# Optimization experiments

Measured on AMD Instinct MI355X. Metric: run time of the kernel, lower is better.

## Reference

```python
import jax, jax.numpy as jnp
import numpy as np

N_NODES = 20000
N_EDGES = 320000
L = 128
NODE_IN = 30
EDGE_IN = 4
NUM_LAYERS = 5


def _mlp(x, w1, b1, a, w2, b2):
    # Linear -> PReLU(scalar slope) -> Linear
    h = x @ w1 + b1
    h = jnp.where(h > 0, h, a * h)
    return h @ w2 + b2


def setup_inputs() -> dict:
    key = jax.random.key(0)
    ks = iter(jax.random.split(key, 64))
    s = 0.02

    def w(shape):
        return (s * jax.random.normal(next(ks), shape)).astype(jnp.float32)

    inp = {}
    inp["x"] = jax.random.normal(next(ks), (N_NODES, NODE_IN), dtype=jnp.float32)
    inp["edge_attr"] = jax.random.normal(next(ks), (N_EDGES, EDGE_IN), dtype=jnp.float32)
    inp["edge_index"] = jax.random.randint(next(ks), (2, N_EDGES), 0, N_NODES, dtype=jnp.int32)
    # node encoder
    inp["ne_w1"] = w((NODE_IN, L)); inp["ne_b1"] = jnp.zeros((L,), jnp.float32)
    inp["ne_a"] = jnp.float32(0.25)
    inp["ne_w2"] = w((L, L)); inp["ne_b2"] = jnp.zeros((L,), jnp.float32)
    # edge encoder
    inp["ee_w1"] = w((EDGE_IN, L)); inp["ee_b1"] = jnp.zeros((L,), jnp.float32)
    inp["ee_a"] = jnp.float32(0.25)
    inp["ee_w2"] = w((L, L)); inp["ee_b2"] = jnp.zeros((L,), jnp.float32)
    # processor layers (stacked over NUM_LAYERS)
    inp["le_w1"] = w((NUM_LAYERS, 3 * L, L)); inp["le_b1"] = jnp.zeros((NUM_LAYERS, L), jnp.float32)
    inp["le_a"] = jnp.full((NUM_LAYERS,), 0.25, jnp.float32)
    inp["le_w2"] = w((NUM_LAYERS, L, L)); inp["le_b2"] = jnp.zeros((NUM_LAYERS, L), jnp.float32)
    inp["ln_w1"] = w((NUM_LAYERS, 2 * L, L)); inp["ln_b1"] = jnp.zeros((NUM_LAYERS, L), jnp.float32)
    inp["ln_a"] = jnp.full((NUM_LAYERS,), 0.25, jnp.float32)
    inp["ln_w2"] = w((NUM_LAYERS, L, L)); inp["ln_b2"] = jnp.zeros((NUM_LAYERS, L), jnp.float32)
    # decoder
    inp["de_w1"] = w((L, L)); inp["de_b1"] = jnp.zeros((L,), jnp.float32)
    inp["de_a"] = jnp.float32(0.25)
    inp["de_w2"] = w((L, 3)); inp["de_b2"] = jnp.zeros((3,), jnp.float32)
    return inp


def reference(x, edge_attr, edge_index,
              ne_w1, ne_b1, ne_a, ne_w2, ne_b2,
              ee_w1, ee_b1, ee_a, ee_w2, ee_b2,
              le_w1, le_b1, le_a, le_w2, le_b2,
              ln_w1, ln_b1, ln_a, ln_w2, ln_b2,
              de_w1, de_b1, de_a, de_w2, de_b2):
    n = x.shape[0]
    src = edge_index[0]  # x_j (source)
    dst = edge_index[1]  # x_i (target), aggregation index

    h = _mlp(x, ne_w1, ne_b1, ne_a, ne_w2, ne_b2)            # [N, L]
    e = _mlp(edge_attr, ee_w1, ee_b1, ee_a, ee_w2, ee_b2)    # [E, L]

    for l in range(le_w1.shape[0]):
        m = jnp.concatenate([h[dst], h[src], e], axis=-1)    # [E, 3L]
        m = _mlp(m, le_w1[l], le_b1[l], le_a[l], le_w2[l], le_b2[l])  # [E, L]
        agg = jax.ops.segment_sum(m, dst, num_segments=n)    # [N, L]
        upd = _mlp(jnp.concatenate([h, agg], axis=-1),
                   ln_w1[l], ln_b1[l], ln_a[l], ln_w2[l], ln_b2[l])
        h = h + upd

    return _mlp(h, de_w1, de_b1, de_a, de_w2, de_b2)         # [N, 3]
```

## Files before the change

### kernel.cpp

```cpp
#include <hip/hip_runtime.h>
#include <cstdint>
#include <cstddef>


#define DEVI static __device__ __forceinline__

typedef __bf16 bf16_t;
typedef bf16_t bf16x8 __attribute__((ext_vector_type(8)));
typedef bf16_t bf16x4 __attribute__((ext_vector_type(4)));
typedef float f32x4v __attribute__((ext_vector_type(4)));

DEVI float4 ld4(const float* p) { return *(const float4*)p; }
DEVI void st4(float* p, float4 v) { *(float4*)p = v; }
DEVI float prelu1(float z, float a) { return z > 0.f ? z : a * z; }
DEVI void atomicAddF(float* p, float v) {
  __hip_atomic_fetch_add(p, v, __ATOMIC_RELAXED, __HIP_MEMORY_SCOPE_AGENT);
}
DEVI f32x4v mfma_bf16(bf16x8 a, bf16x8 b, f32x4v c) {
  return __builtin_amdgcn_mfma_f32_16x16x32_bf16(a, b, c, 0, 0, 0);
}
DEVI void mfma3(f32x4v& acc, bf16x8 ah, bf16x8 al, bf16x8 bh, bf16x8 bl) {
  acc = mfma_bf16(ah, bh, acc);
  acc = mfma_bf16(al, bh, acc);
  acc = mfma_bf16(ah, bl, acc);
}
DEVI void split2(float x, bf16_t& h, bf16_t& l) {
  h = (bf16_t)x;
  l = (bf16_t)(x - (float)h);
}
DEVI bf16x8 ldb8(const bf16_t* p) { return *(const bf16x8*)p; }

#define NST 136
#define EST 72


DEVI void stage_f32(const float* __restrict__ src, int row0, int M,
                    int lane, int wave, bf16_t* SAh, bf16_t* SAl)
{
  const int row = wave * 16 + (lane >> 2);
  const int grow = row0 + row;
  const int colbase = (lane & 3) * 32;
  #pragma unroll
  for (int j = 0; j < 8; ++j) {
    int kc = colbase + j * 4;
    float4 v = make_float4(0.f, 0.f, 0.f, 0.f);
    if (grow < M) v = ld4(src + (size_t)grow * 128 + kc);
    bf16_t h0,l0,h1,l1,h2,l2,h3,l3;
    split2(v.x,h0,l0); split2(v.y,h1,l1); split2(v.z,h2,l2); split2(v.w,h3,l3);
    *(bf16x4*)(SAh + row * NST + kc) = (bf16x4){h0,h1,h2,h3};
    *(bf16x4*)(SAl + row * NST + kc) = (bf16x4){l0,l1,l2,l3};
  }
}

DEVI void stage_planes(const bf16_t* __restrict__ gh, const bf16_t* __restrict__ gl,
                       int row0, int M, int lane, int wave,
                       bf16_t* SAh, bf16_t* SAl)
{
  const int row = wave * 16 + (lane >> 2);
  const int grow = row0 + row;
  const int colbase = (lane & 3) * 32;
  #pragma unroll
  for (int j = 0; j < 4; ++j) {
    int kc = colbase + j * 8;
    bf16x8 vh = {};
    bf16x8 vl = {};
    if (grow < M) {
      vh = ldb8(gh + (size_t)grow * 128 + kc);
      vl = ldb8(gl + (size_t)grow * 128 + kc);
    }
    *(bf16x8*)(SAh + row * NST + kc) = vh;
    *(bf16x8*)(SAl + row * NST + kc) = vl;
  }
}

DEVI void gemm_lds(const bf16_t* SAh, const bf16_t* SAl,
                   const bf16_t* __restrict__ BT, f32x4v acc[8],
                   int wave, int p, int q)
{
  #pragma unroll
  for (int ks = 0; ks < 4; ++ks) {
    const int k0 = ks * 32 + q * 8;
    bf16x8 aH = ldb8(SAh + (wave * 16 + p) * NST + k0);
    bf16x8 aL = ldb8(SAl + (wave * 16 + p) * NST + k0);
    #pragma unroll
    for (int nt = 0; nt < 8; ++nt) {
      const bf16_t* bp = BT + (size_t)(nt * 16 + p) * 128 + k0;
      mfma3(acc[nt], aH, aL, ldb8(bp), ldb8(bp + 16384));
    }
  }
}

DEVI void store_c(float* __restrict__ O, int row0, int M,
                  const f32x4v acc[8], int wave, int p, int q)
{
  int rb = row0 + wave * 16 + q * 4;
  #pragma unroll
  for (int r = 0; r < 4; ++r) {
    if (rb + r < M) {
      float* op = O + (size_t)(rb + r) * 128 + p * 8;
      st4(op,     make_float4(acc[0][r], acc[1][r], acc[2][r], acc[3][r]));
      st4(op + 4, make_float4(acc[4][r], acc[5][r], acc[6][r], acc[7][r]));
    }
  }
}

DEVI void stage_cregs(const f32x4v acc[8], int wave, int p, int q,
                      bf16_t* SAh, bf16_t* SAl)
{
  #pragma unroll
  for (int r = 0; r < 4; ++r) {
    int row = wave * 16 + q * 4 + r;
    bf16x8 vh, vl;
    #pragma unroll
    for (int nt = 0; nt < 8; ++nt) {
      bf16_t hb, lb;
      split2(acc[nt][r], hb, lb);
      vh[nt] = hb; vl[nt] = lb;
    }
    *(bf16x8*)(SAh + row * NST + p * 8) = vh;
    *(bf16x8*)(SAl + row * NST + p * 8) = vl;
  }
}

DEVI void planes_out(bf16_t* __restrict__ gh, bf16_t* __restrict__ gl,
                     int row0, int M, int lane, int wave,
                     const bf16_t* SAh, const bf16_t* SAl)
{
  const int row = wave * 16 + (lane >> 2);
  const int grow = row0 + row;
  const int colbase = (lane & 3) * 32;
  if (grow < M) {
    #pragma unroll
    for (int j = 0; j < 4; ++j) {
      int kc = colbase + j * 8;
      *(bf16x8*)(gh + (size_t)grow * 128 + kc) = *(const bf16x8*)(SAh + row * NST + kc);
      *(bf16x8*)(gl + (size_t)grow * 128 + kc) = *(const bf16x8*)(SAl + row * NST + kc);
    }
  }
}

DEVI void ld8f(float dst[8], const float* __restrict__ src, int p) {
  *(float4*)(dst)     = ld4(src + p * 8);
  *(float4*)(dst + 4) = ld4(src + p * 8 + 4);
}

__global__ __launch_bounds__(128, 2) void k_svu(
    float* Sbuf,
    bf16_t* __restrict__ hSh, bf16_t* __restrict__ hSl,
    const bf16_t* __restrict__ WtilT, const bf16_t* __restrict__ Wn1aT,
    const bf16_t* __restrict__ lnw2T, const bf16_t* __restrict__ W1nextT,
    const float* __restrict__ ln_b1_l, const float* __restrict__ btil_l,
    const int* __restrict__ deg, const float* __restrict__ ln_a_l,
    const float* __restrict__ ln_b2_l,
    float* __restrict__ P, float* __restrict__ Q, int doPQ, int M)
{
  __shared__ __align__(16) bf16_t SAh[32 * NST];
  __shared__ __align__(16) bf16_t SAl[32 * NST];
  const int t = threadIdx.x, lane = t & 63, wave = t >> 6;
  const int p = lane & 15, q = lane >> 4;
  const int row0 = blockIdx.x * 32;

  f32x4v acc1[8];
  #pragma unroll
  for (int j = 0; j < 8; ++j) acc1[j] = (f32x4v){0.f, 0.f, 0.f, 0.f};

  stage_f32(Sbuf, row0, M, lane, wave, SAh, SAl);
  {
    const int row = wave * 16 + (lane >> 2);
    const int grow = row0 + row;
    const int colbase = (lane & 3) * 32;
    if (grow < M) {
      float4 z4 = make_float4(0.f, 0.f, 0.f, 0.f);
      #pragma unroll
      for (int j = 0; j < 8; ++j)
        st4(Sbuf + (size_t)grow * 128 + colbase + j * 4, z4);
    }
  }
  gemm_lds(SAh, SAl, WtilT, acc1, wave, p, q);
  stage_planes(hSh, hSl, row0, M, lane, wave, SAh, SAl);
  gemm_lds(SAh, SAl, Wn1aT, acc1, wave, p, q);

  float hold[8][4];
  #pragma unroll
  for (int r = 0; r < 4; ++r) {
    int row = wave * 16 + q * 4 + r;
    bf16x8 vh = *(const bf16x8*)(SAh + row * NST + p * 8);
    bf16x8 vl = *(const bf16x8*)(SAl + row * NST + p * 8);
    #pragma unroll
    for (int nt = 0; nt < 8; ++nt)
      hold[nt][r] = (float)vh[nt] + (float)vl[nt];
  }
  const float alpha = *ln_a_l;
  float degf[4];
  #pragma unroll
  for (int r = 0; r < 4; ++r) {
    int row = row0 + wave * 16 + q * 4 + r;
    degf[r] = (row < M) ? (float)deg[row] : 0.f;
  }
  float b1c[8], btc[8];
  ld8f(b1c, ln_b1_l, p);
  ld8f(btc, btil_l, p);
  #pragma unroll
  for (int nt = 0; nt < 8; ++nt)
    #pragma unroll
    for (int r = 0; r < 4; ++r)
      acc1[nt][r] = prelu1(acc1[nt][r] + b1c[nt] + degf[r] * btc[nt], alpha);

  stage_cregs(acc1, wave, p, q, SAh, SAl);
  f32x4v acc2[8];
  #pragma unroll
  for (int j = 0; j < 8; ++j) acc2[j] = (f32x4v){0.f, 0.f, 0.f, 0.f};
  gemm_lds(SAh, SAl, lnw2T, acc2, wave, p, q);
  float b2c[8];
  ld8f(b2c, ln_b2_l, p);
  #pragma unroll
  for (int nt = 0; nt < 8; ++nt)
    #pragma unroll
    for (int r = 0; r < 4; ++r)
      acc2[nt][r] = hold[nt][r] + acc2[nt][r] + b2c[nt];

  stage_cregs(acc2, wave, p, q, SAh, SAl);
  planes_out(hSh, hSl, row0, M, lane, wave, SAh, SAl);

  if (doPQ) {
    f32x4v acc3[8];
    #pragma unroll
    for (int j = 0; j < 8; ++j) acc3[j] = (f32x4v){0.f, 0.f, 0.f, 0.f};
    gemm_lds(SAh, SAl, W1nextT, acc3, wave, p, q);
    store_c(P, row0, M, acc3, wave, p, q);
    #pragma unroll
    for (int j = 0; j < 8; ++j) acc3[j] = (f32x4v){0.f, 0.f, 0.f, 0.f};
    gemm_lds(SAh, SAl, W1nextT + 32768, acc3, wave, p, q);
    store_c(Q, row0, M, acc3, wave, p, q);
  }
}

__global__ __launch_bounds__(128, 2) void k_enc(
    const float* __restrict__ UN, const bf16_t* __restrict__ new2T,
    const float* __restrict__ b2, const bf16_t* __restrict__ W1T0,
    bf16_t* __restrict__ hSh, bf16_t* __restrict__ hSl,
    float* __restrict__ P, float* __restrict__ Q, int M)
{
  __shared__ __align__(16) bf16_t SAh[32 * NST];
  __shared__ __align__(16) bf16_t SAl[32 * NST];
  const int t = threadIdx.x, lane = t & 63, wave = t >> 6;
  const int p = lane & 15, q = lane >> 4;
  const int row0 = blockIdx.x * 32;

  f32x4v acc[8];
  #pragma unroll
  for (int j = 0; j < 8; ++j) acc[j] = (f32x4v){0.f, 0.f, 0.f, 0.f};
  stage_f32(UN, row0, M, lane, wave, SAh, SAl);
  gemm_lds(SAh, SAl, new2T, acc, wave, p, q);
  float b2c[8];
  ld8f(b2c, b2, p);
  #pragma unroll
  for (int nt = 0; nt < 8; ++nt)
    #pragma unroll
    for (int r = 0; r < 4; ++r) acc[nt][r] += b2c[nt];
  stage_cregs(acc, wave, p, q, SAh, SAl);
  planes_out(hSh, hSl, row0, M, lane, wave, SAh, SAl);

  f32x4v acc3[8];
  #pragma unroll
  for (int j = 0; j < 8; ++j) acc3[j] = (f32x4v){0.f, 0.f, 0.f, 0.f};
  gemm_lds(SAh, SAl, W1T0, acc3, wave, p, q);
  store_c(P, row0, M, acc3, wave, p, q);
  #pragma unroll
  for (int j = 0; j < 8; ++j) acc3[j] = (f32x4v){0.f, 0.f, 0.f, 0.f};
  gemm_lds(SAh, SAl, W1T0 + 32768, acc3, wave, p, q);
  store_c(Q, row0, M, acc3, wave, p, q);
}

__global__ __launch_bounds__(256, 3) void k_edge(
    const float* __restrict__ sEa, const int* __restrict__ sSrc,
    const int* __restrict__ sDst,
    const int* __restrict__ rowStart, const int* __restrict__ deg,
    const float* __restrict__ ee_w1, const float* __restrict__ ee_b1,
    const float* __restrict__ ee_a,
    const bf16_t* __restrict__ WhatT, const float* __restrict__ bvec,
    const float* __restrict__ alpha_ptr,
    const float* __restrict__ P, const float* __restrict__ Q,
    float* __restrict__ S, int N, int E)
{
  __shared__ __align__(16) float Stile[32 * 132];
  __shared__ __align__(16) float ew[640];
  __shared__ __align__(16) bf16_t Ast[128 * EST];

  const int t = threadIdx.x, lane = t & 63, wave = t >> 6;
  const int p = lane & 15, q = lane >> 4;
  const int e0 = blockIdx.x * 128;
  const int dstLo = sDst[e0];

  for (int i = t; i < 640; i += 256)
    ew[i] = (i < 512) ? ee_w1[i] : ee_b1[i - 512];
  for (int i = t; i < 32 * 132; i += 256) Stile[i] = 0.f;
  __syncthreads();

  const float ua = *ee_a;
  const float alpha = *alpha_ptr;
  float bvc[8];
  ld8f(bvc, bvec, p);

  const int srow = wave * 32 + (lane >> 1);
  const int scb = (lane & 1) * 32;
  float4 eav = make_float4(0.f, 0.f, 0.f, 0.f);
  {
    int ed = e0 + srow;
    if (ed < E) eav = ld4(sEa + (size_t)ed * 4);
  }

  f32x4v acc[2][8];
  #pragma unroll
  for (int i = 0; i < 2; ++i)
    #pragma unroll
    for (int j = 0; j < 8; ++j) acc[i][j] = (f32x4v){0.f, 0.f, 0.f, 0.f};

  for (int c = 0; c < 2; ++c) {
    #pragma unroll
    for (int j = 0; j < 8; ++j) {
      int kc = scb + j * 4;
      int kg = c * 64 + kc;
      float4 w0 = ld4(ew + kg);
      float4 w1 = ld4(ew + 128 + kg);
      float4 w2 = ld4(ew + 256 + kg);
      float4 w3 = ld4(ew + 384 + kg);
      float4 bb = ld4(ew + 512 + kg);
      float ux = bb.x, uy = bb.y, uz = bb.z, uw = bb.w;
      ux = fmaf(eav.x, w0.x, ux); uy = fmaf(eav.x, w0.y, uy);
      uz = fmaf(eav.x, w0.z, uz); uw = fmaf(eav.x, w0.w, uw);
      ux = fmaf(eav.y, w1.x, ux); uy = fmaf(eav.y, w1.y, uy);
      uz = fmaf(eav.y, w1.z, uz); uw = fmaf(eav.y, w1.w, uw);
      ux = fmaf(eav.z, w2.x, ux); uy = fmaf(eav.z, w2.y, uy);
      uz = fmaf(eav.z, w2.z, uz); uw = fmaf(eav.z, w2.w, uw);
      ux = fmaf(eav.w, w3.x, ux); uy = fmaf(eav.w, w3.y, uy);
      uz = fmaf(eav.w, w3.z, uz); uw = fmaf(eav.w, w3.w, uw);
      *(bf16x4*)(Ast + srow * EST + kc) = (bf16x4){
          (bf16_t)prelu1(ux, ua), (bf16_t)prelu1(uy, ua),
          (bf16_t)prelu1(uz, ua), (bf16_t)prelu1(uw, ua)};
    }
    #pragma unroll
    for (int ks = 0; ks < 2; ++ks) {
      const int k0 = ks * 32 + q * 8;
      const int kg = c * 64 + k0;
      bf16x8 aH0 = ldb8(Ast + (wave * 32 + p) * EST + k0);
      bf16x8 aH1 = ldb8(Ast + (wave * 32 + 16 + p) * EST + k0);
      #pragma unroll
      for (int nt = 0; nt < 8; ++nt) {
        const bf16_t* bp = WhatT + (size_t)(nt * 16 + p) * 128 + kg;
        bf16x8 bH = ldb8(bp);
        bf16x8 bL = ldb8(bp + 16384);
        acc[0][nt] = mfma_bf16(aH0, bH, acc[0][nt]);
        acc[0][nt] = mfma_bf16(aH0, bL, acc[0][nt]);
        acc[1][nt] = mfma_bf16(aH1, bH, acc[1][nt]);
        acc[1][nt] = mfma_bf16(aH1, bL, acc[1][nt]);
      }
    }
  }

  #pragma unroll
  for (int mt = 0; mt < 2; ++mt) {
    float rs[8];
    #pragma unroll
    for (int nt = 0; nt < 8; ++nt) rs[nt] = 0.f;
    int curd = -1;
    float pv[8];
    #pragma unroll
    for (int nt = 0; nt < 8; ++nt) pv[nt] = 0.f;
    #pragma unroll
    for (int r = 0; r < 4; ++r) {
      int ed = e0 + wave * 32 + mt * 16 + q * 4 + r;
      if (ed < E) {
        int d = sDst[ed];
        int s = sSrc[ed];
        if (d != curd) {
          if (curd >= 0) {
            int rr = curd - dstLo;
            if (rr < 32) {
              #pragma unroll
              for (int nt = 0; nt < 8; ++nt)
                atomicAdd(&Stile[rr * 132 + p * 8 + nt], rs[nt]);
            } else {
              #pragma unroll
              for (int nt = 0; nt < 8; ++nt)
                atomicAddF(S + (size_t)curd * 128 + p * 8 + nt, rs[nt]);
            }
            #pragma unroll
            for (int nt = 0; nt < 8; ++nt) rs[nt] = 0.f;
          }
          curd = d;
          ld8f(pv, P + (size_t)d * 128, p);
          #pragma unroll
          for (int nt = 0; nt < 8; ++nt) pv[nt] += bvc[nt];
        }
        float qv[8];
        ld8f(qv, Q + (size_t)s * 128, p);
        #pragma unroll
        for (int nt = 0; nt < 8; ++nt) {
          float z = acc[mt][nt][r] + pv[nt] + qv[nt];
          rs[nt] += prelu1(z, alpha);
        }
      }
    }
    if (curd >= 0) {
      int rr = curd - dstLo;
      if (rr < 32) {
        #pragma unroll
        for (int nt = 0; nt < 8; ++nt)
          atomicAdd(&Stile[rr * 132 + p * 8 + nt], rs[nt]);
      } else {
        #pragma unroll
        for (int nt = 0; nt < 8; ++nt)
          atomicAddF(S + (size_t)curd * 128 + p * 8 + nt, rs[nt]);
      }
    }
  }
  __syncthreads();

  const int lastE = (e0 + 127 < E) ? (e0 + 127) : (E - 1);
  const int dstHi = sDst[lastE];
  const int col4 = (t & 31) * 4;
  #pragma unroll
  for (int rr0 = 0; rr0 < 32; rr0 += 8) {
    int rr = rr0 + (t >> 5);
    int d = dstLo + rr;
    if (d <= dstHi && d < N) {
      float4 v = ld4(&Stile[rr * 132 + col4]);
      bool interior = (rowStart[d] >= e0) && (rowStart[d] + deg[d] <= e0 + 128);
      float* sp = S + (size_t)d * 128 + col4;
      if (interior) {
        st4(sp, v);
      } else {
        atomicAddF(sp + 0, v.x); atomicAddF(sp + 1, v.y);
        atomicAddF(sp + 2, v.z); atomicAddF(sp + 3, v.w);
      }
    }
  }
}

__global__ __launch_bounds__(128, 4) void k_dec(
    const bf16_t* __restrict__ hSh, const bf16_t* __restrict__ hSl,
    const bf16_t* __restrict__ dw1T,
    const float* __restrict__ de_b1, const float* __restrict__ de_a,
    const float* __restrict__ de_w2, const float* __restrict__ de_b2,
    float* __restrict__ out, int M)
{
  __shared__ __align__(16) float Cs[32][132];
  __shared__ __align__(16) float w2s[384];
  const int t = threadIdx.x, lane = t & 63, wave = t >> 6;
  const int p = lane & 15, q = lane >> 4;
  const int row0 = blockIdx.x * 32;
  for (int i = t; i < 384; i += 128) w2s[i] = de_w2[i];

  f32x4v acc[8];
  #pragma unroll
  for (int j = 0; j < 8; ++j) acc[j] = (f32x4v){0.f, 0.f, 0.f, 0.f};
  const size_t ra = (size_t)(row0 + wave * 16 + p) * 128;
  #pragma unroll
  for (int ks = 0; ks < 4; ++ks) {
    const int k0 = ks * 32 + q * 8;
    bf16x8 aH = ldb8(hSh + ra + k0);
    bf16x8 aL = ldb8(hSl + ra + k0);
    #pragma unroll
    for (int nt = 0; nt < 8; ++nt) {
      const bf16_t* bp = dw1T + (size_t)(nt * 16 + p) * 128 + k0;
      mfma3(acc[nt], aH, aL, ldb8(bp), ldb8(bp + 16384));
    }
  }
  const float alpha = *de_a;
  float b1c[8];
  ld8f(b1c, de_b1, p);
  #pragma unroll
  for (int r = 0; r < 4; ++r) {
    int row = wave * 16 + q * 4 + r;
    float* cp = &Cs[row][p * 8];
    st4(cp, make_float4(prelu1(acc[0][r] + b1c[0], alpha),
                        prelu1(acc[1][r] + b1c[1], alpha),
                        prelu1(acc[2][r] + b1c[2], alpha),
                        prelu1(acc[3][r] + b1c[3], alpha)));
    st4(cp + 4, make_float4(prelu1(acc[4][r] + b1c[4], alpha),
                            prelu1(acc[5][r] + b1c[5], alpha),
                            prelu1(acc[6][r] + b1c[6], alpha),
                            prelu1(acc[7][r] + b1c[7], alpha)));
  }
  __syncthreads();
  if (t < 32) {
    float s0 = de_b2[0], s1 = de_b2[1], s2 = de_b2[2];
    for (int k = 0; k < 128; ++k) {
      float vv = Cs[t][k];
      s0 = fmaf(vv, w2s[k * 3 + 0], s0);
      s1 = fmaf(vv, w2s[k * 3 + 1], s1);
      s2 = fmaf(vv, w2s[k * 3 + 2], s2);
    }
    int row = row0 + t;
    if (row < M) {
      out[(size_t)row * 3 + 0] = s0;
      out[(size_t)row * 3 + 1] = s1;
      out[(size_t)row * 3 + 2] = s2;
    }
  }
}

__global__ __launch_bounds__(256) void k_tsplit(
    const float* __restrict__ ne_w2, const float* __restrict__ de_w1,
    const float* __restrict__ le_w1, const float* __restrict__ ln_w1,
    const float* __restrict__ ln_w2, bf16_t* __restrict__ WT)
{
  int jid = blockIdx.x;
  const float* src; int slot;
  if (jid == 0)      { src = ne_w2; slot = 0; }
  else if (jid == 1) { src = de_w1; slot = 1; }
  else {
    int l = (jid - 2) >> 2, wj = (jid - 2) & 3;
    slot = 2 + l * 6 + wj;
    src = (wj == 0) ? le_w1 + (size_t)l * 49152
        : (wj == 1) ? le_w1 + (size_t)l * 49152 + 16384
        : (wj == 2) ? ln_w1 + (size_t)l * 32768
                    : ln_w2 + (size_t)l * 16384;
  }
  bf16_t* oh = WT + (size_t)slot * 32768;
  bf16_t* ol = oh + 16384;
  for (int idx = threadIdx.x; idx < 16384; idx += 256) {
    int k = idx >> 7, n = idx & 127;
    bf16_t hb, lb;
    split2(src[idx], hb, lb);
    int pos = ((n & 7) * 16 + (n >> 3)) * 128 + k;
    oh[pos] = hb;
    ol[pos] = lb;
  }
}

__global__ __launch_bounds__(256) void k_fold(
    const float* __restrict__ ee_w2, const float* __restrict__ ee_b2,
    const float* __restrict__ le_w1, const float* __restrict__ le_b1,
    const float* __restrict__ le_w2, const float* __restrict__ le_b2,
    const float* __restrict__ ln_w1,
    bf16_t* __restrict__ WT, float* __restrict__ bvec, float* __restrict__ btil)
{
  const int l = blockIdx.x;
  const int which = blockIdx.y;
  const int z = blockIdx.z;
  const float* L; const float* Rm; const float* lb; const float* badd;
  int slot; float* bout;
  if (which == 0) {
    L = ee_w2; Rm = le_w1 + (size_t)l * 49152 + 256 * 128;
    lb = ee_b2; badd = le_b1 + l * 128;
    slot = 2 + l * 6 + 4; bout = bvec + l * 128;
  } else {
    L = le_w2 + (size_t)l * 16384; Rm = ln_w1 + (size_t)l * 32768 + 128 * 128;
    lb = le_b2 + l * 128; badd = nullptr;
    slot = 2 + l * 6 + 5; bout = btil + l * 128;
  }
  bf16_t* oh = WT + (size_t)slot * 32768;
  bf16_t* ol = oh + 16384;
  const int t = threadIdx.x;
  const int base = z * 2048;
  for (int eidx = base + t; eidx < base + 2048; eidx += 256) {
    int k = eidx >> 7, n = eidx & 127;
    float a = 0.f;
    for (int d = 0; d < 128; d += 4) {
      float4 lv = ld4(L + k * 128 + d);
      a = fmaf(lv.x, Rm[(d + 0) * 128 + n], a);
      a = fmaf(lv.y, Rm[(d + 1) * 128 + n], a);
      a = fmaf(lv.z, Rm[(d + 2) * 128 + n], a);
      a = fmaf(lv.w, Rm[(d + 3) * 128 + n], a);
    }
    bf16_t hb, lbv;
    split2(a, hb, lbv);
    int pos = ((n & 7) * 16 + (n >> 3)) * 128 + k;
    oh[pos] = hb;
    ol[pos] = lbv;
  }
  if (z == 0 && t < 128) {
    float a = badd ? badd[t] : 0.f;
    for (int d = 0; d < 128; ++d) a = fmaf(lb[d], Rm[d * 128 + t], a);
    bout[t] = a;
  }
}

__global__ __launch_bounds__(256) void k_node_u(
    const float* __restrict__ x, const float* __restrict__ w1,
    const float* __restrict__ b1, const float* __restrict__ a_ptr,
    float* __restrict__ U, int M)
{
  int gid = blockIdx.x * 256 + threadIdx.x;
  int m = gid >> 5;
  if (m >= M) return;
  int nc = (gid & 31) << 2;
  float a = *a_ptr;
  float4 bb = ld4(b1 + nc);
  float z0 = bb.x, z1 = bb.y, z2 = bb.z, z3 = bb.w;
  const float* xr = x + (size_t)m * 30;
  #pragma unroll
  for (int j = 0; j < 30; ++j) {
    float xv = xr[j];
    float4 wv = ld4(w1 + j * 128 + nc);
    z0 = fmaf(xv, wv.x, z0); z1 = fmaf(xv, wv.y, z1);
    z2 = fmaf(xv, wv.z, z2); z3 = fmaf(xv, wv.w, z3);
  }
  st4(U + (size_t)m * 128 + nc,
      make_float4(prelu1(z0, a), prelu1(z1, a), prelu1(z2, a), prelu1(z3, a)));
}

__global__ void k_hist(const int* __restrict__ dstIdx, int* __restrict__ deg, int E) {
  int i = blockIdx.x * 256 + threadIdx.x;
  if (i < E) atomicAdd(deg + dstIdx[i], 1);
}

__global__ __launch_bounds__(1024) void k_scan(
    const int* __restrict__ deg, int* __restrict__ cursor,
    int* __restrict__ rowStart, int N, int per)
{
  __shared__ int part[1024];
  const int t = threadIdx.x;
  const int base = t * per;
  int local = 0;
  for (int i = 0; i < per; ++i) {
    int idx = base + i;
    if (idx < N) local += deg[idx];
  }
  part[t] = local;
  __syncthreads();
  for (int off = 1; off < 1024; off <<= 1) {
    int v = (t >= off) ? part[t - off] : 0;
    __syncthreads();
    part[t] += v;
    __syncthreads();
  }
  int run = (t == 0) ? 0 : part[t - 1];
  for (int i = 0; i < per; ++i) {
    int idx = base + i;
    if (idx < N) {
      cursor[idx] = run;
      rowStart[idx] = run;
      run += deg[idx];
    }
  }
}

__global__ void k_scatter(const int* __restrict__ srcIdx, const int* __restrict__ dstIdx,
                          const float* __restrict__ ea, int* __restrict__ cursor,
                          int* __restrict__ sSrc, int* __restrict__ sDst,
                          float* __restrict__ sEa, int E)
{
  int e = blockIdx.x * 256 + threadIdx.x;
  if (e < E) {
    int d = dstIdx[e];
    int p = atomicAdd(cursor + d, 1);
    sSrc[p] = srcIdx[e];
    sDst[p] = d;
    st4(sEa + (size_t)p * 4, ld4(ea + (size_t)e * 4));
  }
}

extern "C" void kernel_launch(void* const* d_in, const int* in_sizes, int n_in,
                              void* d_out, int out_size, void* d_ws, size_t ws_size,
                              hipStream_t stream)
{
  const float* x     = (const float*)d_in[0];
  const float* ea    = (const float*)d_in[1];
  const int*   ei    = (const int*)  d_in[2];
  const float* ne_w1 = (const float*)d_in[3];
  const float* ne_b1 = (const float*)d_in[4];
  const float* ne_a  = (const float*)d_in[5];
  const float* ne_w2 = (const float*)d_in[6];
  const float* ne_b2 = (const float*)d_in[7];
  const float* ee_w1 = (const float*)d_in[8];
  const float* ee_b1 = (const float*)d_in[9];
  const float* ee_a  = (const float*)d_in[10];
  const float* ee_w2 = (const float*)d_in[11];
  const float* ee_b2 = (const float*)d_in[12];
  const float* le_w1 = (const float*)d_in[13];
  const float* le_b1 = (const float*)d_in[14];
  const float* le_a  = (const float*)d_in[15];
  const float* le_w2 = (const float*)d_in[16];
  const float* le_b2 = (const float*)d_in[17];
  const float* ln_w1 = (const float*)d_in[18];
  const float* ln_b1 = (const float*)d_in[19];
  const float* ln_a  = (const float*)d_in[20];
  const float* ln_w2 = (const float*)d_in[21];
  const float* ln_b2 = (const float*)d_in[22];
  const float* de_w1 = (const float*)d_in[23];
  const float* de_b1 = (const float*)d_in[24];
  const float* de_a  = (const float*)d_in[25];
  const float* de_w2 = (const float*)d_in[26];
  const float* de_b2 = (const float*)d_in[27];

  const int N = in_sizes[0] / 30;
  const int E = in_sizes[1] / 4;
  const int* srcIdx = ei;
  const int* dstIdx = ei + E;

  const int g32 = (N + 31) / 32;
  const int gE  = (E + 127) / 128;
  const int Np = g32 * 32;
  const size_t NNp = (size_t)Np * 128;

  float* w = (float*)d_ws;
  float* Pb   = w; w += NNp;
  float* Qb   = w; w += NNp;
  float* Sb   = w; w += NNp;
  float* bvec = w; w += 5 * 128;
  float* btil = w; w += 5 * 128;
  float* sEa  = w; w += (size_t)E * 4;
  bf16_t* hSh = (bf16_t*)w;
  bf16_t* hSl = hSh + NNp;  w += NNp;
  bf16_t* WT  = (bf16_t*)w; w += 32 * 32768 / 2;
  int* ip     = (int*)w;
  int* deg    = ip; ip += N;
  int* cursor = ip; ip += N;
  int* rowStart = ip; ip += N;
  int* sSrc   = ip; ip += E;
  int* sDst   = ip; ip += E;

  float* out = (float*)d_out;

  k_tsplit<<<dim3(22), dim3(256), 0, stream>>>(ne_w2, de_w1, le_w1, ln_w1, ln_w2, WT);
  k_fold<<<dim3(5, 2, 8), dim3(256), 0, stream>>>(ee_w2, ee_b2, le_w1, le_b1,
                                                  le_w2, le_b2, ln_w1, WT, bvec, btil);
  hipMemsetAsync(deg, 0, (size_t)N * 4, stream);
  k_hist<<<dim3((E + 255) / 256), dim3(256), 0, stream>>>(dstIdx, deg, E);
  k_scan<<<dim3(1), dim3(1024), 0, stream>>>(deg, cursor, rowStart, N,
                                             (N + 1023) / 1024);
  k_scatter<<<dim3((E + 255) / 256), dim3(256), 0, stream>>>(
      srcIdx, dstIdx, ea, cursor, sSrc, sDst, sEa, E);

  k_node_u<<<dim3((N * 32 + 255) / 256), dim3(256), 0, stream>>>(x, ne_w1, ne_b1, ne_a, Sb, N);
  k_enc<<<dim3(g32), dim3(128), 0, stream>>>(Sb, WT, ne_b2, WT + 2 * 32768,
                                             hSh, hSl, Pb, Qb, N);

  hipMemsetAsync(Sb, 0, (size_t)N * 128 * 4, stream);

  for (int l = 0; l < 5; ++l) {
    const bf16_t* slotL = WT + (size_t)(2 + l * 6) * 32768;
    k_edge<<<dim3(gE), dim3(256), 0, stream>>>(
        sEa, sSrc, sDst, rowStart, deg, ee_w1, ee_b1, ee_a,
        slotL + 4 * 32768, bvec + l * 128, le_a + l, Pb, Qb, Sb, N, E);
    const bf16_t* W1next = (l < 4) ? (WT + (size_t)(2 + (l + 1) * 6) * 32768) : WT;
    k_svu<<<dim3(g32), dim3(128), 0, stream>>>(
        Sb, hSh, hSl, slotL + 5 * 32768, slotL + 2 * 32768, slotL + 3 * 32768,
        W1next, ln_b1 + (size_t)l * 128, btil + l * 128, deg, ln_a + l,
        ln_b2 + (size_t)l * 128, Pb, Qb, (l < 4) ? 1 : 0, N);
  }

  k_dec<<<dim3(g32), dim3(128), 0, stream>>>(hSh, hSl, WT + 32768, de_b1, de_a,
                                             de_w2, de_b2, out, N);
}
```

Baseline: 1.396 ms.

## Split node-update GEMM columns across four waves per 32-row block

The node-update and encoder kernels move from 2 waves (each owning 16 rows and all 128 output columns) to 4 waves, where each wave owns 16 rows and half of the output columns. Accumulator count per thread halves, and the staging, store and LDS split helpers are rewritten for the half-width layout. Because waves now share rows in LDS, __syncthreads barriers are added between staging and GEMM phases. The aim is more wave parallelism and lower register pressure on the node-side kernels, at the cost of extra barriers and each wave reloading its A fragments.

```diff
diff --git a/kernel.cpp b/kernel.cpp
--- a/kernel.cpp
+++ b/kernel.cpp
@@ -34,14 +34,14 @@
 #define EST 72
 
 
-DEVI void stage_f32(const float* __restrict__ src, int row0, int M,
-                    int lane, int wave, bf16_t* SAh, bf16_t* SAl)
-{
-  const int row = wave * 16 + (lane >> 2);
+DEVI void stage_f32_c4(const float* __restrict__ src, int row0, int M,
+                       int lane, int h, int cH, bf16_t* SAh, bf16_t* SAl)
+{
+  const int row = h * 16 + (lane >> 2);
   const int grow = row0 + row;
-  const int colbase = (lane & 3) * 32;
-  #pragma unroll
-  for (int j = 0; j < 8; ++j) {
+  const int colbase = cH * 64 + (lane & 3) * 16;
+  #pragma unroll
+  for (int j = 0; j < 4; ++j) {
     int kc = colbase + j * 4;
     float4 v = make_float4(0.f, 0.f, 0.f, 0.f);
     if (grow < M) v = ld4(src + (size_t)grow * 128 + kc);
@@ -52,15 +52,15 @@
   }
 }
 
-DEVI void stage_planes(const bf16_t* __restrict__ gh, const bf16_t* __restrict__ gl,
-                       int row0, int M, int lane, int wave,
-                       bf16_t* SAh, bf16_t* SAl)
-{
-  const int row = wave * 16 + (lane >> 2);
+DEVI void stage_planes_c4(const bf16_t* __restrict__ gh, const bf16_t* __restrict__ gl,
+                          int row0, int M, int lane, int h, int cH,
+                          bf16_t* SAh, bf16_t* SAl)
+{
+  const int row = h * 16 + (lane >> 2);
   const int grow = row0 + row;
-  const int colbase = (lane & 3) * 32;
-  #pragma unroll
-  for (int j = 0; j < 4; ++j) {
+  const int colbase = cH * 64 + (lane & 3) * 16;
+  #pragma unroll
+  for (int j = 0; j < 2; ++j) {
     int kc = colbase + j * 8;
     bf16x8 vh = {};
     bf16x8 vl = {};
@@ -73,65 +73,64 @@
   }
 }
 
-DEVI void gemm_lds(const bf16_t* SAh, const bf16_t* SAl,
-                   const bf16_t* __restrict__ BT, f32x4v acc[8],
-                   int wave, int p, int q)
+DEVI void gemm_c4(const bf16_t* SAh, const bf16_t* SAl,
+                  const bf16_t* __restrict__ BT, f32x4v acc[4],
+                  int h, int ntb, int p, int q)
 {
   #pragma unroll
   for (int ks = 0; ks < 4; ++ks) {
     const int k0 = ks * 32 + q * 8;
-    bf16x8 aH = ldb8(SAh + (wave * 16 + p) * NST + k0);
-    bf16x8 aL = ldb8(SAl + (wave * 16 + p) * NST + k0);
-    #pragma unroll
-    for (int nt = 0; nt < 8; ++nt) {
-      const bf16_t* bp = BT + (size_t)(nt * 16 + p) * 128 + k0;
+    bf16x8 aH = ldb8(SAh + (h * 16 + p) * NST + k0);
+    bf16x8 aL = ldb8(SAl + (h * 16 + p) * NST + k0);
+    #pragma unroll
+    for (int nt = 0; nt < 4; ++nt) {
+      const bf16_t* bp = BT + (size_t)((ntb + nt) * 16 + p) * 128 + k0;
       mfma3(acc[nt], aH, aL, ldb8(bp), ldb8(bp + 16384));
     }
   }
 }
 
-DEVI void store_c(float* __restrict__ O, int row0, int M,
-                  const f32x4v acc[8], int wave, int p, int q)
-{
-  int rb = row0 + wave * 16 + q * 4;
+DEVI void store_c4(float* __restrict__ O, int row0, int M,
+                   const f32x4v acc[4], int h, int cH, int p, int q)
+{
+  int rb = row0 + h * 16 + q * 4;
   #pragma unroll
   for (int r = 0; r < 4; ++r) {
     if (rb + r < M) {
-      float* op = O + (size_t)(rb + r) * 128 + p * 8;
-      st4(op,     make_float4(acc[0][r], acc[1][r], acc[2][r], acc[3][r]));
-      st4(op + 4, make_float4(acc[4][r], acc[5][r], acc[6][r], acc[7][r]));
-    }
-  }
-}
-
-DEVI void stage_cregs(const f32x4v acc[8], int wave, int p, int q,
-                      bf16_t* SAh, bf16_t* SAl)
+      float* op = O + (size_t)(rb + r) * 128 + p * 8 + cH * 4;
+      st4(op, make_float4(acc[0][r], acc[1][r], acc[2][r], acc[3][r]));
+    }
+  }
+}
+
+DEVI void stage_cregs_c4(const f32x4v acc[4], int h, int cH, int p, int q,
+                         bf16_t* SAh, bf16_t* SAl)
 {
   #pragma unroll
   for (int r = 0; r < 4; ++r) {
-    int row = wave * 16 + q * 4 + r;
-    bf16x8 vh, vl;
-    #pragma unroll
-    for (int nt = 0; nt < 8; ++nt) {
+    int row = h * 16 + q * 4 + r;
+    bf16x4 vh, vl;
+    #pragma unroll
+    for (int nt = 0; nt < 4; ++nt) {
       bf16_t hb, lb;
       split2(acc[nt][r], hb, lb);
       vh[nt] = hb; vl[nt] = lb;
     }
-    *(bf16x8*)(SAh + row * NST + p * 8) = vh;
-    *(bf16x8*)(SAl + row * NST + p * 8) = vl;
-  }
-}
-
-DEVI void planes_out(bf16_t* __restrict__ gh, bf16_t* __restrict__ gl,
-                     int row0, int M, int lane, int wave,
-                     const bf16_t* SAh, const bf16_t* SAl)
-{
-  const int row = wave * 16 + (lane >> 2);
+    *(bf16x4*)(SAh + row * NST + p * 8 + cH * 4) = vh;
+    *(bf16x4*)(SAl + row * NST + p * 8 + cH * 4) = vl;
+  }
+}
+
+DEVI void planes_out_c4(bf16_t* __restrict__ gh, bf16_t* __restrict__ gl,
+                        int row0, int M, int lane, int h, int cH,
+                        const bf16_t* SAh, const bf16_t* SAl)
+{
+  const int row = h * 16 + (lane >> 2);
   const int grow = row0 + row;
-  const int colbase = (lane & 3) * 32;
+  const int colbase = cH * 64 + (lane & 3) * 16;
   if (grow < M) {
     #pragma unroll
-    for (int j = 0; j < 4; ++j) {
+    for (int j = 0; j < 2; ++j) {
       int kc = colbase + j * 8;
       *(bf16x8*)(gh + (size_t)grow * 128 + kc) = *(const bf16x8*)(SAh + row * NST + kc);
       *(bf16x8*)(gl + (size_t)grow * 128 + kc) = *(const bf16x8*)(SAl + row * NST + kc);
@@ -144,7 +143,11 @@
   *(float4*)(dst + 4) = ld4(src + p * 8 + 4);
 }
 
-__global__ __launch_bounds__(128, 2) void k_svu(
+DEVI void ld4f(float dst[4], const float* __restrict__ src, int p, int cH) {
+  *(float4*)(dst) = ld4(src + p * 8 + cH * 4);
+}
+
+__global__ __launch_bounds__(256, 2) void k_svu(
     float* Sbuf,
     bf16_t* __restrict__ hSh, bf16_t* __restrict__ hSl,
     const bf16_t* __restrict__ WtilT, const bf16_t* __restrict__ Wn1aT,
@@ -157,85 +160,95 @@
   __shared__ __align__(16) bf16_t SAh[32 * NST];
   __shared__ __align__(16) bf16_t SAl[32 * NST];
   const int t = threadIdx.x, lane = t & 63, wave = t >> 6;
+  const int h = wave & 1, cH = wave >> 1;
   const int p = lane & 15, q = lane >> 4;
   const int row0 = blockIdx.x * 32;
 
-  f32x4v acc1[8];
-  #pragma unroll
-  for (int j = 0; j < 8; ++j) acc1[j] = (f32x4v){0.f, 0.f, 0.f, 0.f};
-
-  stage_f32(Sbuf, row0, M, lane, wave, SAh, SAl);
+  f32x4v acc1[4];
+  #pragma unroll
+  for (int j = 0; j < 4; ++j) acc1[j] = (f32x4v){0.f, 0.f, 0.f, 0.f};
+
+  stage_f32_c4(Sbuf, row0, M, lane, h, cH, SAh, SAl);
   {
-    const int row = wave * 16 + (lane >> 2);
+    const int row = h * 16 + (lane >> 2);
     const int grow = row0 + row;
-    const int colbase = (lane & 3) * 32;
+    const int colbase = cH * 64 + (lane & 3) * 16;
     if (grow < M) {
       float4 z4 = make_float4(0.f, 0.f, 0.f, 0.f);
       #pragma unroll
-      for (int j = 0; j < 8; ++j)
+      for (int j = 0; j < 4; ++j)
         st4(Sbuf + (size_t)grow * 128 + colbase + j * 4, z4);
     }
   }
-  gemm_lds(SAh, SAl, WtilT, acc1, wave, p, q);
-  stage_planes(hSh, hSl, row0, M, lane, wave, SAh, SAl);
-  gemm_lds(SAh, SAl, Wn1aT, acc1, wave, p, q);
-
-  float hold[8][4];
+  __syncthreads();
+  gemm_c4(SAh, SAl, WtilT, acc1, h, cH * 4, p, q);
+  __syncthreads();
+  stage_planes_c4(hSh, hSl, row0, M, lane, h, cH, SAh, SAl);
+  __syncthreads();
+  gemm_c4(SAh, SAl, Wn1aT, acc1, h, cH * 4, p, q);
+
+  float hold[4][4];
   #pragma unroll
   for (int r = 0; r < 4; ++r) {
-    int row = wave * 16 + q * 4 + r;
-    bf16x8 vh = *(const bf16x8*)(SAh + row * NST + p * 8);
-    bf16x8 vl = *(const bf16x8*)(SAl + row * NST + p * 8);
-    #pragma unroll
-    for (int nt = 0; nt < 8; ++nt)
+    int row = h * 16 + q * 4 + r;
+    bf16x4 vh = *(const bf16x4*)(SAh + row * NST + p * 8 + cH * 4);
+    bf16x4 vl = *(const bf16x4*)(SAl + row * NST + p * 8 + cH * 4);
+    #pragma unroll
+    for (int nt = 0; nt < 4; ++nt)
       hold[nt][r] = (float)vh[nt] + (float)vl[nt];
   }
+  __syncthreads();
+
   const float alpha = *ln_a_l;
   float degf[4];
   #pragma unroll
   for (int r = 0; r < 4; ++r) {
-    int row = row0 + wave * 16 + q * 4 + r;
+    int row = row0 + h * 16 + q * 4 + r;
     degf[r] = (row < M) ? (float)deg[row] : 0.f;
   }
-  float b1c[8], btc[8];
-  ld8f(b1c, ln_b1_l, p);
-  ld8f(btc, btil_l, p);
-  #pragma unroll
-  for (int nt = 0; nt < 8; ++nt)
+  float b1c[4], btc[4];
+  ld4f(b1c, ln_b1_l, p, cH);
+  ld4f(btc, btil_l, p, cH);
+  #pragma unroll
+  for (int nt = 0; nt < 4; ++nt)
     #pragma unroll
     for (int r = 0; r < 4; ++r)
       acc1[nt][r] = prelu1(acc1[nt][r] + b1c[nt] + degf[r] * btc[nt], alpha);
 
-  stage_cregs(acc1, wave, p, q, SAh, SAl);
-  f32x4v acc2[8];
-  #pragma unroll
-  for (int j = 0; j < 8; ++j) acc2[j] = (f32x4v){0.f, 0.f, 0.f, 0.f};
-  gemm_lds(SAh, SAl, lnw2T, acc2, wave, p, q);
-  float b2c[8];
-  ld8f(b2c, ln_b2_l, p);
-  #pragma unroll
-  for (int nt = 0; nt < 8; ++nt)
+  stage_cregs_c4(acc1, h, cH, p, q, SAh, SAl);
+  __syncthreads();
+  f32x4v acc2[4];
+  #pragma unroll
+  for (int j = 0; j < 4; ++j) acc2[j] = (f32x4v){0.f, 0.f, 0.f, 0.f};
+  gemm_c4(SAh, SAl, lnw2T, acc2, h, cH * 4, p, q);
+  __syncthreads();
+
+  float b2c[4];
+  ld4f(b2c, ln_b2_l, p, cH);
+  #pragma unroll
+  for (int nt = 0; nt < 4; ++nt)
     #pragma unroll
     for (int r = 0; r < 4; ++r)
       acc2[nt][r] = hold[nt][r] + acc2[nt][r] + b2c[nt];
 
-  stage_cregs(acc2, wave, p, q, SAh, SAl);
-  planes_out(hSh, hSl, row0, M, lane, wave, SAh, SAl);
+  stage_cregs_c4(acc2, h, cH, p, q, SAh, SAl);
+  __syncthreads();
+  planes_out_c4(hSh, hSl, row0, M, lane, h, cH, SAh, SAl);
 
   if (doPQ) {
-    f32x4v acc3[8];
-    #pragma unroll
-    for (int j = 0; j < 8; ++j) acc3[j] = (f32x4v){0.f, 0.f, 0.f, 0.f};
-    gemm_lds(SAh, SAl, W1nextT, acc3, wave, p, q);
-    store_c(P, row0, M, acc3, wave, p, q);
-    #pragma unroll
-    for (int j = 0; j < 8; ++j) acc3[j] = (f32x4v){0.f, 0.f, 0.f, 0.f};
-    gemm_lds(SAh, SAl, W1nextT + 32768, acc3, wave, p, q);
-    store_c(Q, row0, M, acc3, wave, p, q);
-  }
-}
-
-__global__ __launch_bounds__(128, 2) void k_enc(
+    f32x4v acc3[4];
+    #pragma unroll
+    for (int j = 0; j < 4; ++j) acc3[j] = (f32x4v){0.f, 0.f, 0.f, 0.f};
+    gemm_c4(SAh, SAl, W1nextT, acc3, h, cH * 4, p, q);
+    store_c4(P, row0, M, acc3, h, cH, p, q);
+    #pragma unroll
+    for (int j = 0; j < 4; ++j) acc3[j] = (f32x4v){0.f, 0.f, 0.f, 0.f};
+    gemm_c4(SAh, SAl, W1nextT + 32768, acc3, h, cH * 4, p, q);
+    store_c4(Q, row0, M, acc3, h, cH, p, q);
+  }
+}
+
+__global__ __launch_bounds__(256, 2) void k_enc(
     const float* __restrict__ UN, const bf16_t* __restrict__ new2T,
     const float* __restrict__ b2, const bf16_t* __restrict__ W1T0,
     bf16_t* __restrict__ hSh, bf16_t* __restrict__ hSl,
@@ -244,32 +257,36 @@
   __shared__ __align__(16) bf16_t SAh[32 * NST];
   __shared__ __align__(16) bf16_t SAl[32 * NST];
   const int t = threadIdx.x, lane = t & 63, wave = t >> 6;
+  const int h = wave & 1, cH = wave >> 1;
   const int p = lane & 15, q = lane >> 4;
   const int row0 = blockIdx.x * 32;
 
-  f32x4v acc[8];
-  #pragma unroll
-  for (int j = 0; j < 8; ++j) acc[j] = (f32x4v){0.f, 0.f, 0.f, 0.f};
-  stage_f32(UN, row0, M, lane, wave, SAh, SAl);
-  gemm_lds(SAh, SAl, new2T, acc, wave, p, q);
-  float b2c[8];
-  ld8f(b2c, b2, p);
-  #pragma unroll
-  for (int nt = 0; nt < 8; ++nt)
+  f32x4v acc[4];
+  #pragma unroll
+  for (int j = 0; j < 4; ++j) acc[j] = (f32x4v){0.f, 0.f, 0.f, 0.f};
+  stage_f32_c4(UN, row0, M, lane, h, cH, SAh, SAl);
+  __syncthreads();
+  gemm_c4(SAh, SAl, new2T, acc, h, cH * 4, p, q);
+  __syncthreads();
+  float b2c[4];
+  ld4f(b2c, b2, p, cH);
+  #pragma unroll
+  for (int nt = 0; nt < 4; ++nt)
     #pragma unroll
     for (int r = 0; r < 4; ++r) acc[nt][r] += b2c[nt];
-  stage_cregs(acc, wave, p, q, SAh, SAl);
-  planes_out(hSh, hSl, row0, M, lane, wave, SAh, SAl);
-
-  f32x4v acc3[8];
-  #pragma unroll
-  for (int j = 0; j < 8; ++j) acc3[j] = (f32x4v){0.f, 0.f, 0.f, 0.f};
-  gemm_lds(SAh, SAl, W1T0, acc3, wave, p, q);
-  store_c(P, row0, M, acc3, wave, p, q);
-  #pragma unroll
-  for (int j = 0; j < 8; ++j) acc3[j] = (f32x4v){0.f, 0.f, 0.f, 0.f};
-  gemm_lds(SAh, SAl, W1T0 + 32768, acc3, wave, p, q);
-  store_c(Q, row0, M, acc3, wave, p, q);
+  stage_cregs_c4(acc, h, cH, p, q, SAh, SAl);
+  __syncthreads();
+  planes_out_c4(hSh, hSl, row0, M, lane, h, cH, SAh, SAl);
+
+  f32x4v acc3[4];
+  #pragma unroll
+  for (int j = 0; j < 4; ++j) acc3[j] = (f32x4v){0.f, 0.f, 0.f, 0.f};
+  gemm_c4(SAh, SAl, W1T0, acc3, h, cH * 4, p, q);
+  store_c4(P, row0, M, acc3, h, cH, p, q);
+  #pragma unroll
+  for (int j = 0; j < 4; ++j) acc3[j] = (f32x4v){0.f, 0.f, 0.f, 0.f};
+  gemm_c4(SAh, SAl, W1T0 + 32768, acc3, h, cH * 4, p, q);
+  store_c4(Q, row0, M, acc3, h, cH, p, q);
 }
 
 __global__ __launch_bounds__(256, 3) void k_edge(
@@ -726,7 +743,7 @@
       srcIdx, dstIdx, ea, cursor, sSrc, sDst, sEa, E);
 
   k_node_u<<<dim3((N * 32 + 255) / 256), dim3(256), 0, stream>>>(x, ne_w1, ne_b1, ne_a, Sb, N);
-  k_enc<<<dim3(g32), dim3(128), 0, stream>>>(Sb, WT, ne_b2, WT + 2 * 32768,
+  k_enc<<<dim3(g32), dim3(256), 0, stream>>>(Sb, WT, ne_b2, WT + 2 * 32768,
                                              hSh, hSl, Pb, Qb, N);
 
   hipMemsetAsync(Sb, 0, (size_t)N * 128 * 4, stream);
@@ -737,7 +754,7 @@
         sEa, sSrc, sDst, rowStart, deg, ee_w1, ee_b1, ee_a,
         slotL + 4 * 32768, bvec + l * 128, le_a + l, Pb, Qb, Sb, N, E);
     const bf16_t* W1next = (l < 4) ? (WT + (size_t)(2 + (l + 1) * 6) * 32768) : WT;
-    k_svu<<<dim3(g32), dim3(128), 0, stream>>>(
+    k_svu<<<dim3(g32), dim3(256), 0, stream>>>(
         Sb, hSh, hSl, slotL + 5 * 32768, slotL + 2 * 32768, slotL + 3 * 32768,
         W1next, ln_b1 + (size_t)l * 128, btil + l * 128, deg, ln_a + l,
         ln_b2 + (size_t)l * 128, Pb, Qb, (l < 4) ? 1 : 0, N);
```

Result: faster. 1.368 ms (-2.1%).
